# Performance work log

Hardware: AMD Instinct MI355X
Metric: run time of the kernel (lower is better)

## Reference

```python
import jax, jax.numpy as jnp
import numpy as np

GROUPS = 16
HEADS = 8
GN_EPS = 1e-5
L2_EPS = 1e-12


def setup_inputs() -> dict:
    key = jax.random.key(0)
    ks = jax.random.split(key, 8)
    B, C, H, W = 16, 256, 64, 64
    cg = C // GROUPS  # 16
    x = jax.random.normal(ks[0], (B, C, H, W), dtype=jnp.float32)
    # conv1x1 on grouped channels (has bias by default in nn.Conv2d)
    w_conv1x1 = jax.random.normal(ks[1], (cg, cg), dtype=jnp.float32) * 0.1
    b_conv1x1 = jax.random.normal(ks[2], (cg,), dtype=jnp.float32) * 0.01
    # GroupNorm(cg, cg) affine params
    gn_w = jnp.ones((cg,), dtype=jnp.float32)
    gn_b = jnp.zeros((cg,), dtype=jnp.float32)
    # qkv 1x1 conv (bias=False): [3C, C]
    w_qkv = jax.random.normal(ks[3], (3 * C, C), dtype=jnp.float32) * 0.05
    # project_out 1x1 conv (bias=False): [C, C]
    w_proj = jax.random.normal(ks[4], (C, C), dtype=jnp.float32) * 0.05
    temperature = jnp.ones((HEADS, 1, 1), dtype=jnp.float32)
    return {"x": x, "w_conv1x1": w_conv1x1, "b_conv1x1": b_conv1x1,
            "gn_w": gn_w, "gn_b": gn_b, "w_qkv": w_qkv, "w_proj": w_proj,
            "temperature": temperature}


def _forward(x, w_conv1x1, b_conv1x1, gn_w, gn_b, w_qkv, w_proj, temperature):
    b, c, h, w = x.shape
    g, cg = GROUPS, x.shape[1] // GROUPS
    gx = x.reshape(b * g, cg, h, w)

    # --- coordinate-attention gating branch ---
    x_h = gx.mean(axis=3)                      # [bg, cg, h]
    x_w = gx.mean(axis=2)                      # [bg, cg, w]
    cat = jnp.concatenate([x_h, x_w], axis=2)  # [bg, cg, h+w]
    hw_feat = jnp.einsum('oi,bil->bol', w_conv1x1, cat) + b_conv1x1[None, :, None]
    xh, xw = hw_feat[:, :, :h], hw_feat[:, :, h:]
    x1 = jax.nn.sigmoid(xh)[:, :, :, None] * jax.nn.sigmoid(xw)[:, :, None, :]  # [bg,cg,h,w]
    # GroupNorm(cg, cg) == per-channel normalization over (h, w)
    mu = x1.mean(axis=(2, 3), keepdims=True)
    var = x1.var(axis=(2, 3), keepdims=True)
    x1 = (x1 - mu) * jax.lax.rsqrt(var + GN_EPS)
    x1 = x1 * gn_w[None, :, None, None] + gn_b[None, :, None, None]
    # softmax over channels of global avg pool -> [bg, cg]
    x11 = jax.nn.softmax(x1.mean(axis=(2, 3)), axis=-1)

    # --- normalized channel (Restormer-style) attention ---
    n = h * w
    qkv = jnp.einsum('oi,bin->bon', w_qkv, x.reshape(b, c, n))  # [b, 3c, n]
    q, k, v = jnp.split(qkv, 3, axis=1)
    ch = c // HEADS
    q = q.reshape(b, HEADS, ch, n)
    k = k.reshape(b, HEADS, ch, n)
    v = v.reshape(b, HEADS, ch, n)
    q = q / jnp.maximum(jnp.linalg.norm(q, axis=-1, keepdims=True), L2_EPS)
    k = k / jnp.maximum(jnp.linalg.norm(k, axis=-1, keepdims=True), L2_EPS)
    attn = jnp.einsum('bhcn,bhdn->bhcd', q, k) * temperature[None]  # [b,H,ch,ch]
    attn = jax.nn.softmax(attn, axis=-1)
    out = jnp.einsum('bhcd,bhdn->bhcn', attn, v).reshape(b, c, n)
    out = jnp.einsum('oi,bin->bon', w_proj, out).reshape(b, c, h, w)

    # --- sigmoid-gated residual combine ---
    x12 = out.reshape(b * g, cg, n)
    weights = jnp.einsum('bc,bcn->bn', x11, x12).reshape(b * g, 1, h, w)
    return (gx * jax.nn.sigmoid(weights)).reshape(b, c, h, w) + out


def reference(x, w_conv1x1, b_conv1x1, gn_w, gn_b, w_qkv, w_proj, temperature):
    return _forward(x, w_conv1x1, b_conv1x1, gn_w, gn_b, w_qkv, w_proj, temperature)
```

## Files before the change

kernel.cpp:

```cpp
#include <hip/hip_runtime.h>
#include <math.h>


__device__ __forceinline__ float sigmoidf_(float v) { return 1.0f / (1.0f + __expf(-v)); }

typedef _Float16 half8 __attribute__((ext_vector_type(8)));
typedef _Float16 half4 __attribute__((ext_vector_type(4)));
typedef float f32x4 __attribute__((ext_vector_type(4)));

#define GLOAD_LDS16(gp, lp)                                                     \
    __builtin_amdgcn_global_load_lds(                                           \
        (const __attribute__((address_space(1))) void*)(gp),                    \
        (__attribute__((address_space(3))) void*)(lp), 16, 0, 0)

__global__ __launch_bounds__(256) void prep_fused(
    const float* __restrict__ X, _Float16* __restrict__ Xh, _Float16* __restrict__ Xt)
{
    __shared__ float tl[64][68];
    const int b = blockIdx.z, c0 = blockIdx.y * 64, n0 = blockIdx.x * 64;
    const int t = threadIdx.x;
    const int r0 = t >> 4;
    const int q = (t & 15) * 4;
    const float* Xb = X + ((long)b * 256 + c0) * 4096 + n0;
    _Float16* Xhb = Xh + ((long)b * 256 + c0) * 4096 + n0;
    #pragma unroll
    for (int i = 0; i < 4; ++i) {
        const int r = r0 + i * 16;
        const float4 v = *(const float4*)(Xb + (long)r * 4096 + q);
        tl[r][q + 0] = v.x; tl[r][q + 1] = v.y;
        tl[r][q + 2] = v.z; tl[r][q + 3] = v.w;
        half4 h = { (_Float16)v.x, (_Float16)v.y, (_Float16)v.z, (_Float16)v.w };
        *(half4*)(Xhb + (long)r * 4096 + q) = h;
    }
    __syncthreads();
    const int nn = t >> 2, cc = (t & 3) * 16;
    _Float16* Xtb = Xt + ((long)b * 4096 + n0 + nn) * 256 + c0 + cc;
    half8 o0, o1;
    #pragma unroll
    for (int k = 0; k < 8; ++k) o0[k] = (_Float16)tl[cc + k][nn];
    #pragma unroll
    for (int k = 0; k < 8; ++k) o1[k] = (_Float16)tl[cc + 8 + k][nn];
    *(half8*)(Xtb) = o0;
    *(half8*)(Xtb + 8) = o1;
}

__global__ __launch_bounds__(256) void cvt_half(const float* __restrict__ in,
                                                _Float16* __restrict__ o)
{
    const long i = ((long)blockIdx.x * 256 + threadIdx.x) * 4;
    const float4 v = *(const float4*)(in + i);
    half4 h = { (_Float16)v.x, (_Float16)v.y, (_Float16)v.z, (_Float16)v.w };
    *(half4*)(o + i) = h;
}

__global__ __launch_bounds__(256) void gram_split(const _Float16* __restrict__ Xh,
                                                  float* __restrict__ pG)
{
    __shared__ _Float16 Al[128 * 32];
    __shared__ _Float16 Bl[128 * 32];
    const int hw = blockIdx.x + 2 * blockIdx.y + 4 * blockIdx.z;
    const int f  = (hw & 7) * 64 + (hw >> 3);
    const int bx = f & 1, by = (f >> 1) & 1, bz = f >> 2;
    const int b = bz >> 3, s = bz & 7;
    const int m0 = by * 128, n0 = bx * 128;
    const _Float16* Xb = Xh + (long)b * 256 * 4096;
    const int t = threadIdx.x, lane = t & 63, wv = t >> 6;
    const int wm = (wv >> 1) * 64, wn = (wv & 1) * 64;
    f32x4 acc[4][4] = {};

    const int kbeg = s * 512, kend = kbeg + 512;
    for (int k0 = kbeg; k0 < kend; k0 += 32) {
        __syncthreads();
        #pragma unroll
        for (int r = 0; r < 2; ++r) {
            const int e = (r * 256 + t) * 8;
            const int row = e >> 5, col = e & 31;
            GLOAD_LDS16(Xb + (long)(m0 + row) * 4096 + k0 + col, &Al[e]);
            GLOAD_LDS16(Xb + (long)(n0 + row) * 4096 + k0 + col, &Bl[e]);
        }
        __syncthreads();
        half8 af[4], bf[4];
        #pragma unroll
        for (int ff = 0; ff < 4; ++ff) {
            af[ff] = *(const half8*)&Al[(wm + ff * 16 + (lane & 15)) * 32 + (lane >> 4) * 8];
            bf[ff] = *(const half8*)&Bl[(wn + ff * 16 + (lane & 15)) * 32 + (lane >> 4) * 8];
        }
        #pragma unroll
        for (int i = 0; i < 4; ++i)
            #pragma unroll
            for (int j = 0; j < 4; ++j)
                acc[i][j] = __builtin_amdgcn_mfma_f32_16x16x32_f16(af[i], bf[j], acc[i][j], 0, 0, 0);
    }
    float* pGb = pG + (long)s * 1048576 + (long)b * 65536;
    #pragma unroll
    for (int i = 0; i < 4; ++i)
        #pragma unroll
        for (int j = 0; j < 4; ++j) {
            const int row = m0 + wm + i * 16 + (lane >> 4) * 4;
            const int col = n0 + wn + j * 16 + (lane & 15);
            float* gp = pGb + (long)row * 256 + col;
            #pragma unroll
            for (int r = 0; r < 4; ++r) gp[(long)r * 256] = acc[i][j][r];
        }
}

__global__ __launch_bounds__(256) void reduce_g(const float* __restrict__ pG,
                                                _Float16* __restrict__ Gh)
{
    const long i = ((long)blockIdx.x * 256 + threadIdx.x) * 4;
    f32x4 s = {};
    #pragma unroll
    for (int k = 0; k < 8; ++k) {
        const float4 v = *(const float4*)(pG + (long)k * 1048576 + i);
        s[0] += v.x; s[1] += v.y; s[2] += v.z; s[3] += v.w;
    }
    half4 h = { (_Float16)s[0], (_Float16)s[1], (_Float16)s[2], (_Float16)s[3] };
    *(half4*)(Gh + i) = h;
}

template <bool DIAG, bool F16OUT>
__global__ __launch_bounds__(256) void mfma_bt(
    const _Float16* __restrict__ A, const _Float16* __restrict__ B,
    float* __restrict__ Cf, _Float16* __restrict__ Ch,
    long sA, long sB, long sC)
{
    __shared__ _Float16 Al[128 * 32];
    __shared__ _Float16 Bl[128 * 32];
    const int b = blockIdx.z;
    const int m0 = blockIdx.y * 128;
    const int n0 = DIAG ? m0 : blockIdx.x * 128;
    const _Float16* Ab = A + (long)b * sA;
    const _Float16* Bb = B + (long)b * sB;
    const int t = threadIdx.x, lane = t & 63, wv = t >> 6;
    const int wm = (wv >> 1) * 64, wn = (wv & 1) * 64;
    f32x4 acc[4][4] = {};

    for (int k0 = 0; k0 < 256; k0 += 32) {
        __syncthreads();
        #pragma unroll
        for (int r = 0; r < 2; ++r) {
            const int e = (r * 256 + t) * 8;
            const int row = e >> 5, col = e & 31;
            GLOAD_LDS16(Ab + (long)(m0 + row) * 256 + k0 + col, &Al[e]);
            GLOAD_LDS16(Bb + (long)(n0 + row) * 256 + k0 + col, &Bl[e]);
        }
        __syncthreads();
        half8 af[4], bf[4];
        #pragma unroll
        for (int ff = 0; ff < 4; ++ff) {
            af[ff] = *(const half8*)&Al[(wm + ff * 16 + (lane & 15)) * 32 + (lane >> 4) * 8];
            bf[ff] = *(const half8*)&Bl[(wn + ff * 16 + (lane & 15)) * 32 + (lane >> 4) * 8];
        }
        #pragma unroll
        for (int i = 0; i < 4; ++i)
            #pragma unroll
            for (int j = 0; j < 4; ++j)
                acc[i][j] = __builtin_amdgcn_mfma_f32_16x16x32_f16(af[i], bf[j], acc[i][j], 0, 0, 0);
    }
    #pragma unroll
    for (int i = 0; i < 4; ++i)
        #pragma unroll
        for (int j = 0; j < 4; ++j) {
            const int row = m0 + wm + i * 16 + (lane >> 4) * 4;
            const int col = n0 + wn + j * 16 + (lane & 15);
            #pragma unroll
            for (int r = 0; r < 4; ++r) {
                if (F16OUT)
                    Ch[(long)b * sC + (long)(row + r) * 256 + col] = (_Float16)acc[i][j][r];
                else
                    Cf[(long)b * sC + (long)(row + r) * 256 + col] = acc[i][j][r];
            }
        }
}

__global__ __launch_bounds__(256) void snorm_kernel(
    const _Float16* __restrict__ Th, const _Float16* __restrict__ wqkvh,
    float* __restrict__ Qn)
{
    const int gw = (int)((blockIdx.x * 256 + threadIdx.x) >> 6);
    const int lane = threadIdx.x & 63;
    const int b = gw >> 9, r = gw & 511;
    const half4 a = *(const half4*)(Th + (long)b * 131072 + (long)r * 256 + lane * 4);
    const half4 w = *(const half4*)(wqkvh + (long)r * 256 + lane * 4);
    float s = (float)a[0] * (float)w[0] + (float)a[1] * (float)w[1]
            + (float)a[2] * (float)w[2] + (float)a[3] * (float)w[3];
    #pragma unroll
    for (int off = 32; off; off >>= 1) s += __shfl_xor(s, off, 64);
    if (lane == 0) Qn[(long)b * 512 + r] = s;
}

__global__ __launch_bounds__(256) void attn2_kernel(
    const float* __restrict__ S1, const float* __restrict__ Qn,
    const float* __restrict__ wqkv, const float* __restrict__ temp,
    _Float16* __restrict__ MmT)
{
    const int bh = blockIdx.x;
    const int b = bh >> 3, h = bh & 7;
    const int t = threadIdx.x;
    __shared__ float pa[32][36];
    __shared__ float qn[32], kn[32];

    {
        const int r = t >> 3, c4 = (t & 7) * 4;
        const float4 v = *(const float4*)(
            S1 + (long)b * 65536 + (long)(h * 32 + r) * 256 + h * 32 + c4);
        pa[r][c4 + 0] = v.x; pa[r][c4 + 1] = v.y;
        pa[r][c4 + 2] = v.z; pa[r][c4 + 3] = v.w;
    }
    if (t < 32)
        qn[t] = fmaxf(sqrtf(Qn[(long)b * 512 + h * 32 + t]), 1e-12f);
    else if (t < 64)
        kn[t - 32] = fmaxf(sqrtf(Qn[(long)b * 512 + 256 + h * 32 + (t - 32)]), 1e-12f);
    __syncthreads();

    if (t < 32) {
        const float qin = temp[h] / qn[t];
        float lg[32];
        float mx = -1e30f;
        #pragma unroll
        for (int d = 0; d < 32; ++d) {
            const float l = pa[t][d] * qin / kn[d];
            lg[d] = l;
            mx = fmaxf(mx, l);
        }
        float s = 0.f;
        #pragma unroll
        for (int d = 0; d < 32; ++d) { lg[d] = __expf(lg[d] - mx); s += lg[d]; }
        const float inv = 1.0f / s;
        #pragma unroll
        for (int d = 0; d < 32; ++d) pa[t][d] = lg[d] * inv;
    }
    __syncthreads();

    float accm[32];
    #pragma unroll
    for (int c = 0; c < 32; ++c) accm[c] = 0.f;
    const float* wvp = wqkv + (long)(512 + h * 32) * 256 + t;
    #pragma unroll 4
    for (int d = 0; d < 32; ++d) {
        const float wvv = wvp[(long)d * 256];
        #pragma unroll
        for (int c = 0; c < 32; ++c) accm[c] += pa[c][d] * wvv;
    }
    _Float16* mo = MmT + (long)b * 65536 + (long)t * 256 + h * 32;
    #pragma unroll
    for (int c = 0; c < 32; ++c) mo[c] = (_Float16)accm[c];
}

__global__ __launch_bounds__(256) void w2h_kernel(
    const _Float16* __restrict__ Ph, const float* __restrict__ gnb,
    _Float16* __restrict__ W2)
{
    const int b = blockIdx.x, i = threadIdx.x;
    float e[16];
    float mx = -1e30f;
    #pragma unroll
    for (int c = 0; c < 16; ++c) mx = fmaxf(mx, gnb[c]);
    float s = 0.f;
    #pragma unroll
    for (int c = 0; c < 16; ++c) { e[c] = __expf(gnb[c] - mx); s += e[c]; }
    const float inv = 1.0f / s;
    const _Float16* Pb = Ph + (long)b * 65536 + i;
    #pragma unroll
    for (int g = 0; g < 16; ++g) {
        float acc = 0.f;
        #pragma unroll
        for (int c = 0; c < 16; ++c) acc += e[c] * (float)Pb[(long)(g * 16 + c) * 256];
        W2[((long)b * 16 + g) * 256 + i] = (_Float16)(acc * inv);
    }
}

__global__ __launch_bounds__(256) void out_fused(
    const _Float16* __restrict__ Ph, const _Float16* __restrict__ Xt,
    const _Float16* __restrict__ Xh, const _Float16* __restrict__ W2h,
    float* __restrict__ out)
{
    __shared__ __align__(16) char smem[40960];
    float (*cst)[128] = (float(*)[128])smem;
    float (*S2l)[128] = (float(*)[128])(smem + 32768);

    const int hw = blockIdx.x + 32 * blockIdx.y + 64 * blockIdx.z;
    const int f  = (hw & 7) * 128 + (hw >> 3);
    const int bx = f & 31, by = (f >> 5) & 1, bz = f >> 6;

    const int b = bz;
    const int m0 = by * 128, n0 = bx * 128;
    const _Float16* Ab = Ph + (long)b * 65536;
    const _Float16* Bb = Xt + (long)b * 1048576;
    const _Float16* W2b = W2h + (long)b * 4096;
    const int t = threadIdx.x, lane = t & 63, wv = t >> 6;
    const int wm = (wv >> 1) * 64, wn = (wv & 1) * 64;

    f32x4 acc[4][4] = {};
    f32x4 s2acc[4] = {};

#define OF_STAGE(P, K0) do {                                                     \
        _Float16* Al_ = (_Float16*)(smem + (P) * 16384);                         \
        _Float16* Bl_ = (_Float16*)(smem + (P) * 16384 + 8192);                  \
        _Pragma("unroll")                                                        \
        for (int r_ = 0; r_ < 2; ++r_) {                                         \
            const int e_ = (r_ * 256 + t) * 8;                                   \
            const int row_ = e_ >> 5, col_ = e_ & 31;                            \
            GLOAD_LDS16(Ab + (long)(m0 + row_) * 256 + (K0) + col_, &Al_[e_]);   \
            GLOAD_LDS16(Bb + (long)(n0 + row_) * 256 + (K0) + col_, &Bl_[e_]);   \
        } } while (0)

    OF_STAGE(0, 0);
    __syncthreads();
    int cur = 0;
    for (int ks = 0; ks < 8; ++ks) {
        if (ks < 7) OF_STAGE(cur ^ 1, (ks + 1) * 32);
        const int k0 = ks * 32;
        const half8 wf = *(const half8*)(W2b + (long)(lane & 15) * 256 + k0 + (lane >> 4) * 8);
        const _Float16* Al = (const _Float16*)(smem + cur * 16384);
        const _Float16* Bl = (const _Float16*)(smem + cur * 16384 + 8192);
        half8 af[4], bf[4];
        #pragma unroll
        for (int ff = 0; ff < 4; ++ff) {
            af[ff] = *(const half8*)&Al[(wm + ff * 16 + (lane & 15)) * 32 + (lane >> 4) * 8];
            bf[ff] = *(const half8*)&Bl[(wn + ff * 16 + (lane & 15)) * 32 + (lane >> 4) * 8];
        }
        #pragma unroll
        for (int i = 0; i < 4; ++i)
            #pragma unroll
            for (int j = 0; j < 4; ++j)
                acc[i][j] = __builtin_amdgcn_mfma_f32_16x16x32_f16(af[i], bf[j], acc[i][j], 0, 0, 0);
        #pragma unroll
        for (int j = 0; j < 4; ++j)
            s2acc[j] = __builtin_amdgcn_mfma_f32_16x16x32_f16(wf, bf[j], s2acc[j], 0, 0, 0);
        __syncthreads();
        cur ^= 1;
    }
#undef OF_STAGE

    if (wm == 0) {
        #pragma unroll
        for (int j = 0; j < 4; ++j)
            #pragma unroll
            for (int r = 0; r < 4; ++r)
                S2l[(lane >> 4) * 4 + r][wn + j * 16 + (lane & 15)] = s2acc[j][r];
    }

    const _Float16* Xhb = Xh + (long)b * 1048576;
    float* ob = out + (long)b * 1048576;

    #pragma unroll
    for (int hf = 0; hf < 2; ++hf) {
        if (wm == hf * 64) {
            #pragma unroll
            for (int i = 0; i < 4; ++i)
                #pragma unroll
                for (int j = 0; j < 4; ++j)
                    #pragma unroll
                    for (int r = 0; r < 4; ++r)
                        cst[i * 16 + (lane >> 4) * 4 + r][wn + j * 16 + (lane & 15)] = acc[i][j][r];
        }
        __syncthreads();
        #pragma unroll
        for (int it = 0; it < 8; ++it) {
            const int row = it * 8 + (t >> 5);
            const int col = (t & 31) * 4;
            const int c = m0 + hf * 64 + row;
            const float4 v = *(const float4*)&cst[row][col];
            const float4 s2 = *(const float4*)&S2l[c >> 4][col];
            const half4 xv = *(const half4*)(Xhb + (long)c * 4096 + n0 + col);
            float4 o;
            o.x = (float)xv[0] * sigmoidf_(s2.x) + v.x;
            o.y = (float)xv[1] * sigmoidf_(s2.y) + v.y;
            o.z = (float)xv[2] * sigmoidf_(s2.z) + v.z;
            o.w = (float)xv[3] * sigmoidf_(s2.w) + v.w;
            *(float4*)(ob + (long)c * 4096 + n0 + col) = o;
        }
        __syncthreads();
    }
}

template <bool BT, bool EPI>
__global__ __launch_bounds__(256) void gemm64(
    const float* __restrict__ A, const float* __restrict__ B, float* __restrict__ C,
    int M, int N, int K, long sA, long sB, long sC,
    const float* __restrict__ X, const float* __restrict__ WP)
{
    __shared__ float As[32][68];
    __shared__ float Bs[32][68];
    const int b = blockIdx.z;
    const float* Ab = A + (long)b * sA;
    const float* Bb = B + (long)b * sB;
    float* Cb = C + (long)b * sC;
    const int t = threadIdx.x;
    const int tx = t & 15, ty = t >> 4;
    const int m0 = blockIdx.y * 64, n0 = blockIdx.x * 64;

    float acc[4][4] = {};

    for (int k0 = 0; k0 < K; k0 += 32) {
        __syncthreads();
        #pragma unroll
        for (int f0 = 0; f0 < 512; f0 += 256) {
            const int f1 = f0 + t;
            const int row = f1 >> 3, c4 = f1 & 7;
            const float4 v = *(const float4*)(Ab + (long)(m0 + row) * K + k0 + c4 * 4);
            As[c4 * 4 + 0][row] = v.x;
            As[c4 * 4 + 1][row] = v.y;
            As[c4 * 4 + 2][row] = v.z;
            As[c4 * 4 + 3][row] = v.w;
        }
        if (BT) {
            #pragma unroll
            for (int f0 = 0; f0 < 512; f0 += 256) {
                const int f1 = f0 + t;
                const int row = f1 >> 3, c4 = f1 & 7;
                const float4 v = *(const float4*)(Bb + (long)(n0 + row) * K + k0 + c4 * 4);
                Bs[c4 * 4 + 0][row] = v.x;
                Bs[c4 * 4 + 1][row] = v.y;
                Bs[c4 * 4 + 2][row] = v.z;
                Bs[c4 * 4 + 3][row] = v.w;
            }
        } else {
            #pragma unroll
            for (int f0 = 0; f0 < 512; f0 += 256) {
                const int f1 = f0 + t;
                const int kk = f1 >> 4, c4 = f1 & 15;
                *(float4*)&Bs[kk][c4 * 4] =
                    *(const float4*)(Bb + (long)(k0 + kk) * N + n0 + c4 * 4);
            }
        }
        __syncthreads();
        #pragma unroll
        for (int kk = 0; kk < 32; ++kk) {
            const float4 av = *(const float4*)&As[kk][ty * 4];
            const float4 bv = *(const float4*)&Bs[kk][tx * 4];
            const float a0 = av.x, a1 = av.y, a2 = av.z, a3 = av.w;
            const float b0 = bv.x, b1 = bv.y, b2 = bv.z, b3 = bv.w;
            acc[0][0] += a0 * b0; acc[0][1] += a0 * b1; acc[0][2] += a0 * b2; acc[0][3] += a0 * b3;
            acc[1][0] += a1 * b0; acc[1][1] += a1 * b1; acc[1][2] += a1 * b2; acc[1][3] += a1 * b3;
            acc[2][0] += a2 * b0; acc[2][1] += a2 * b1; acc[2][2] += a2 * b2; acc[2][3] += a2 * b3;
            acc[3][0] += a3 * b0; acc[3][1] += a3 * b1; acc[3][2] += a3 * b2; acc[3][3] += a3 * b3;
        }
    }

    if (EPI) {
        #pragma unroll
        for (int i = 0; i < 4; ++i) {
            const int c = m0 + ty * 4 + i;
            const long nidx = n0 + tx * 4;
            const float4 xv = *(const float4*)(X + ((long)b * 256 + c) * 4096 + nidx);
            const float4 wv = *(const float4*)(WP + ((long)b * 16 + (c >> 4)) * 4096 + nidx);
            float4 o;
            o.x = xv.x * sigmoidf_(wv.x) + acc[i][0];
            o.y = xv.y * sigmoidf_(wv.y) + acc[i][1];
            o.z = xv.z * sigmoidf_(wv.z) + acc[i][2];
            o.w = xv.w * sigmoidf_(wv.w) + acc[i][3];
            *(float4*)(Cb + (long)c * N + nidx) = o;
        }
    } else {
        #pragma unroll
        for (int i = 0; i < 4; ++i) {
            const float4 o = make_float4(acc[i][0], acc[i][1], acc[i][2], acc[i][3]);
            *(float4*)(Cb + (long)(m0 + ty * 4 + i) * N + n0 + tx * 4) = o;
        }
    }
}

__global__ __launch_bounds__(256) void attn_kernel(
    const float* __restrict__ T, const float* __restrict__ wqkv,
    const float* __restrict__ temp, float* __restrict__ Mout, long tStride)
{
    const int bh = blockIdx.x;
    const int b = bh >> 3, h = bh & 7;
    const int t = threadIdx.x;
    __shared__ float Tq[32][260];
    __shared__ float qk[32][33];
    __shared__ float qn[32], kn[32];
    const float* Tb = T + (long)b * tStride;

    for (int f = t; f < 32 * 64; f += 256) {
        const int r = f >> 6, c4 = f & 63;
        *(float4*)&Tq[r][c4 * 4] = *(const float4*)(Tb + (long)(h * 32 + r) * 256 + c4 * 4);
    }
    __syncthreads();

    if (t < 32) {
        float s = 0.f;
        const float* wq = wqkv + (long)(h * 32 + t) * 256;
        #pragma unroll 4
        for (int k = 0; k < 256; k += 4) {
            const float4 a = *(const float4*)&Tq[t][k];
            const float4 w = *(const float4*)(wq + k);
            s += a.x * w.x + a.y * w.y + a.z * w.z + a.w * w.w;
        }
        qn[t] = fmaxf(sqrtf(s), 1e-12f);
    } else if (t < 64) {
        const int d = t - 32;
        float s = 0.f;
        const float* tk = Tb + (long)(256 + h * 32 + d) * 256;
        const float* wk = wqkv + (long)(256 + h * 32 + d) * 256;
        #pragma unroll 4
        for (int k = 0; k < 256; k += 4) {
            const float4 a = *(const float4*)(tk + k);
            const float4 w = *(const float4*)(wk + k);
            s += a.x * w.x + a.y * w.y + a.z * w.z + a.w * w.w;
        }
        kn[d] = fmaxf(sqrtf(s), 1e-12f);
    }

    {
        const int c = t >> 3, d0 = (t & 7) * 4;
        float s0 = 0, s1 = 0, s2 = 0, s3 = 0;
        const float* wk0 = wqkv + (long)(256 + h * 32 + d0) * 256;
        #pragma unroll 4
        for (int k = 0; k < 256; k += 4) {
            const float4 a = *(const float4*)&Tq[c][k];
            const float4 w0 = *(const float4*)(wk0 + k);
            const float4 w1 = *(const float4*)(wk0 + 256 + k);
            const float4 w2 = *(const float4*)(wk0 + 512 + k);
            const float4 w3 = *(const float4*)(wk0 + 768 + k);
            s0 += a.x * w0.x + a.y * w0.y + a.z * w0.z + a.w * w0.w;
            s1 += a.x * w1.x + a.y * w1.y + a.z * w1.z + a.w * w1.w;
            s2 += a.x * w2.x + a.y * w2.y + a.z * w2.z + a.w * w2.w;
            s3 += a.x * w3.x + a.y * w3.y + a.z * w3.z + a.w * w3.w;
        }
        qk[c][d0 + 0] = s0;
        qk[c][d0 + 1] = s1;
        qk[c][d0 + 2] = s2;
        qk[c][d0 + 3] = s3;
    }
    __syncthreads();

    if (t < 32) {
        const float tscale = temp[h];
        const float qin = tscale / qn[t];
        float lg[32];
        float mx = -1e30f;
        #pragma unroll
        for (int d = 0; d < 32; ++d) {
            const float l = qk[t][d] * qin / kn[d];
            lg[d] = l;
            mx = fmaxf(mx, l);
        }
        float s = 0.f;
        #pragma unroll
        for (int d = 0; d < 32; ++d) { lg[d] = __expf(lg[d] - mx); s += lg[d]; }
        const float inv = 1.0f / s;
        #pragma unroll
        for (int d = 0; d < 32; ++d) qk[t][d] = lg[d] * inv;
    }
    __syncthreads();

    float accm[32];
    #pragma unroll
    for (int c = 0; c < 32; ++c) accm[c] = 0.f;
    const float* wvp = wqkv + (long)(512 + h * 32) * 256 + t;
    #pragma unroll 4
    for (int d = 0; d < 32; ++d) {
        const float wvv = wvp[(long)d * 256];
        #pragma unroll
        for (int c = 0; c < 32; ++c) accm[c] += qk[c][d] * wvv;
    }
    float* mo = Mout + (long)b * 256 * 256 + (long)(h * 32) * 256 + t;
    #pragma unroll
    for (int c = 0; c < 32; ++c) mo[(long)c * 256] = accm[c];
}

__global__ __launch_bounds__(256) void w2_kernel(
    const float* __restrict__ P, const float* __restrict__ gnb, float* __restrict__ W2)
{
    const int b = blockIdx.x, i = threadIdx.x;
    float e[16];
    float mx = -1e30f;
    #pragma unroll
    for (int c = 0; c < 16; ++c) mx = fmaxf(mx, gnb[c]);
    float s = 0.f;
    #pragma unroll
    for (int c = 0; c < 16; ++c) { e[c] = __expf(gnb[c] - mx); s += e[c]; }
    const float inv = 1.0f / s;
    const float* Pb = P + (long)b * 256 * 256 + i;
    #pragma unroll
    for (int g = 0; g < 16; ++g) {
        float acc = 0.f;
        #pragma unroll
        for (int c = 0; c < 16; ++c) acc += e[c] * Pb[(long)(g * 16 + c) * 256];
        W2[((long)b * 16 + g) * 256 + i] = acc * inv;
    }
}

__global__ __launch_bounds__(256) void wpre_kernel(
    const float* __restrict__ W2, const float* __restrict__ X, float* __restrict__ WP)
{
    __shared__ float w2s[16][260];
    const int b = blockIdx.y;
    const int n = blockIdx.x * 256 + threadIdx.x;
    for (int f = threadIdx.x; f < 16 * 64; f += 256) {
        const int g = f >> 6, c4 = f & 63;
        *(float4*)&w2s[g][c4 * 4] = *(const float4*)(W2 + ((long)b * 16 + g) * 256 + c4 * 4);
    }
    __syncthreads();
    float acc[16] = {};
    const float* xb = X + (long)b * 256 * 4096 + n;
    for (int k = 0; k < 256; ++k) {
        const float xv = xb[(long)k * 4096];
        #pragma unroll
        for (int g = 0; g < 16; ++g) acc[g] += w2s[g][k] * xv;
    }
    #pragma unroll
    for (int g = 0; g < 16; ++g) WP[((long)b * 16 + g) * 4096 + n] = acc[g];
}

extern "C" void kernel_launch(void* const* d_in, const int* in_sizes, int n_in,
                              void* d_out, int out_size, void* d_ws, size_t ws_size,
                              hipStream_t stream)
{
    const float* x     = (const float*)d_in[0];
    const float* gnb   = (const float*)d_in[4];
    const float* wqkv  = (const float*)d_in[5];
    const float* wproj = (const float*)d_in[6];
    const float* temp  = (const float*)d_in[7];
    float* out = (float*)d_out;

    if (ws_size >= 82051072ULL) {
        char* w = (char*)d_ws;
        _Float16* Xh = (_Float16*)w;
        _Float16* Xt = (_Float16*)(w + 33554432);
        float*    S1 = (float*)(w + 67108864);
        char*     pool = w + 71303168;
        _Float16* wqkvh  = (_Float16*)pool;
        _Float16* wprojh = (_Float16*)(pool + 393216);
        _Float16* Gh     = (_Float16*)(pool + 524288);
        _Float16* MmT    = (_Float16*)(pool + 524288);
        _Float16* Th     = (_Float16*)(pool + 2621440);
        float*    Qn     = (float*)(pool + 6815744);
        _Float16* Ph     = (_Float16*)(pool + 6848512);
        _Float16* W2h    = (_Float16*)(pool + 8945664);
        float*    pG     = (float*)d_out;

        prep_fused<<<dim3(64, 4, 16), 256, 0, stream>>>(x, Xh, Xt);
        cvt_half<<<192, 256, 0, stream>>>(wqkv, wqkvh);
        cvt_half<<<64, 256, 0, stream>>>(wproj, wprojh);
        gram_split<<<dim3(2, 2, 128), 256, 0, stream>>>(Xh, pG);
        reduce_g<<<1024, 256, 0, stream>>>(pG, Gh);
        mfma_bt<false, true><<<dim3(2, 4, 16), 256, 0, stream>>>(
            wqkvh, Gh, nullptr, Th, 0L, 65536L, 131072L);
        snorm_kernel<<<2048, 256, 0, stream>>>(Th, wqkvh, Qn);
        mfma_bt<true, false><<<dim3(1, 2, 16), 256, 0, stream>>>(
            Th, wqkvh + 65536, S1, nullptr, 131072L, 0L, 65536L);
        attn2_kernel<<<128, 256, 0, stream>>>(S1, Qn, wqkv, temp, MmT);
        mfma_bt<false, true><<<dim3(2, 2, 16), 256, 0, stream>>>(
            wprojh, MmT, nullptr, Ph, 0L, 65536L, 65536L);
        w2h_kernel<<<16, 256, 0, stream>>>(Ph, gnb, W2h);
        out_fused<<<dim3(32, 2, 16), 256, 0, stream>>>(Ph, Xt, Xh, W2h, out);
    } else {
        float* ws = (float*)d_ws;
        float* G  = ws;
        float* T  = G  + 16L * 65536;
        float* Mm = T  + 16L * 196608;
        float* P  = Mm + 16L * 65536;
        float* W2 = P  + 16L * 65536;
        float* WP = W2 + 16L * 4096;

        gemm64<true, false><<<dim3(4, 4, 16), 256, 0, stream>>>(
            x, x, G, 256, 256, 4096, 1048576L, 1048576L, 65536L, nullptr, nullptr);
        gemm64<false, false><<<dim3(4, 12, 16), 256, 0, stream>>>(
            wqkv, G, T, 768, 256, 256, 0L, 65536L, 196608L, nullptr, nullptr);
        attn_kernel<<<128, 256, 0, stream>>>(T, wqkv, temp, Mm, 196608L);
        gemm64<false, false><<<dim3(4, 4, 16), 256, 0, stream>>>(
            wproj, Mm, P, 256, 256, 256, 0L, 65536L, 65536L, nullptr, nullptr);
        w2_kernel<<<16, 256, 0, stream>>>(P, gnb, W2);
        wpre_kernel<<<dim3(16, 16), 256, 0, stream>>>(W2, x, WP);
        gemm64<false, true><<<dim3(64, 4, 16), 256, 0, stream>>>(
            P, x, out, 256, 4096, 256, 65536L, 1048576L, 1048576L, x, WP);
    }
}
```

Before: 123.3 us.

## Exploit Gram symmetry, merge weight casts, fold norm calc into attention kernel

The Gram split kernel now computes only three of the four 128x128 tiles, since X·Xᵀ is symmetric, and a new mirror kernel fills the missing lower-left block by transposing the upper-right one. The two weight conversion launches are merged into one, and the separate q/k squared-norm kernel is removed; attn2 now computes those norms itself from Th and the half-precision weights. The final output uses nontemporal stores. Together these cut Gram MFMA work by a quarter and drop launches, at the cost of an extra small transpose launch and more work per attention block.

Measured after the change: 121.4 us. About the same (-1.5%).

```diff
diff --git a/kernel.cpp b/kernel.cpp
--- a/kernel.cpp
+++ b/kernel.cpp
@@ -44,13 +44,22 @@
     *(half8*)(Xtb + 8) = o1;
 }
 
-__global__ __launch_bounds__(256) void cvt_half(const float* __restrict__ in,
-                                                _Float16* __restrict__ o)
-{
-    const long i = ((long)blockIdx.x * 256 + threadIdx.x) * 4;
-    const float4 v = *(const float4*)(in + i);
-    half4 h = { (_Float16)v.x, (_Float16)v.y, (_Float16)v.z, (_Float16)v.w };
-    *(half4*)(o + i) = h;
+__global__ __launch_bounds__(256) void cvt_weights(
+    const float* __restrict__ wqkv, const float* __restrict__ wproj,
+    _Float16* __restrict__ wqkvh, _Float16* __restrict__ wprojh)
+{
+    const int blk = blockIdx.x;
+    if (blk < 192) {
+        const long i = ((long)blk * 256 + threadIdx.x) * 4;
+        const float4 v = *(const float4*)(wqkv + i);
+        half4 h = { (_Float16)v.x, (_Float16)v.y, (_Float16)v.z, (_Float16)v.w };
+        *(half4*)(wqkvh + i) = h;
+    } else {
+        const long i = ((long)(blk - 192) * 256 + threadIdx.x) * 4;
+        const float4 v = *(const float4*)(wproj + i);
+        half4 h = { (_Float16)v.x, (_Float16)v.y, (_Float16)v.z, (_Float16)v.w };
+        *(half4*)(wprojh + i) = h;
+    }
 }
 
 __global__ __launch_bounds__(256) void gram_split(const _Float16* __restrict__ Xh,
@@ -58,11 +67,13 @@
 {
     __shared__ _Float16 Al[128 * 32];
     __shared__ _Float16 Bl[128 * 32];
-    const int hw = blockIdx.x + 2 * blockIdx.y + 4 * blockIdx.z;
-    const int f  = (hw & 7) * 64 + (hw >> 3);
-    const int bx = f & 1, by = (f >> 1) & 1, bz = f >> 2;
+    const int hw = blockIdx.x + 3 * blockIdx.y;
+    const int f  = (hw & 7) * 48 + (hw >> 3);
+    const int tile = f % 3;
+    const int bz = f / 3;
     const int b = bz >> 3, s = bz & 7;
-    const int m0 = by * 128, n0 = bx * 128;
+    const int m0 = (tile == 1) ? 128 : 0;
+    const int n0 = (tile == 0) ? 0 : 128;
     const _Float16* Xb = Xh + (long)b * 256 * 4096;
     const int t = threadIdx.x, lane = t & 63, wv = t >> 6;
     const int wm = (wv >> 1) * 64, wn = (wv & 1) * 64;
@@ -116,6 +127,25 @@
     }
     half4 h = { (_Float16)s[0], (_Float16)s[1], (_Float16)s[2], (_Float16)s[3] };
     *(half4*)(Gh + i) = h;
+}
+
+__global__ __launch_bounds__(256) void mirror_g(_Float16* __restrict__ Gh)
+{
+    __shared__ _Float16 tl[64][72];
+    const int b = blockIdx.z, r0 = 128 + blockIdx.y * 64, c0 = blockIdx.x * 64;
+    const int t = threadIdx.x;
+    const int ii = t >> 2, jj = (t & 3) * 16;
+    _Float16* Gb = Gh + (long)b * 65536;
+    *(half8*)&tl[ii][jj]     = *(const half8*)(Gb + (long)(c0 + ii) * 256 + r0 + jj);
+    *(half8*)&tl[ii][jj + 8] = *(const half8*)(Gb + (long)(c0 + ii) * 256 + r0 + jj + 8);
+    __syncthreads();
+    half8 o0, o1;
+    #pragma unroll
+    for (int k = 0; k < 8; ++k) o0[k] = tl[jj + k][ii];
+    #pragma unroll
+    for (int k = 0; k < 8; ++k) o1[k] = tl[jj + 8 + k][ii];
+    *(half8*)(Gb + (long)(r0 + ii) * 256 + c0 + jj) = o0;
+    *(half8*)(Gb + (long)(r0 + ii) * 256 + c0 + jj + 8) = o1;
 }
 
 template <bool DIAG, bool F16OUT>
@@ -173,26 +203,10 @@
         }
 }
 
-__global__ __launch_bounds__(256) void snorm_kernel(
-    const _Float16* __restrict__ Th, const _Float16* __restrict__ wqkvh,
-    float* __restrict__ Qn)
-{
-    const int gw = (int)((blockIdx.x * 256 + threadIdx.x) >> 6);
-    const int lane = threadIdx.x & 63;
-    const int b = gw >> 9, r = gw & 511;
-    const half4 a = *(const half4*)(Th + (long)b * 131072 + (long)r * 256 + lane * 4);
-    const half4 w = *(const half4*)(wqkvh + (long)r * 256 + lane * 4);
-    float s = (float)a[0] * (float)w[0] + (float)a[1] * (float)w[1]
-            + (float)a[2] * (float)w[2] + (float)a[3] * (float)w[3];
-    #pragma unroll
-    for (int off = 32; off; off >>= 1) s += __shfl_xor(s, off, 64);
-    if (lane == 0) Qn[(long)b * 512 + r] = s;
-}
-
 __global__ __launch_bounds__(256) void attn2_kernel(
-    const float* __restrict__ S1, const float* __restrict__ Qn,
-    const float* __restrict__ wqkv, const float* __restrict__ temp,
-    _Float16* __restrict__ MmT)
+    const float* __restrict__ S1, const _Float16* __restrict__ Th,
+    const _Float16* __restrict__ wqkvh, const float* __restrict__ wqkv,
+    const float* __restrict__ temp, _Float16* __restrict__ MmT)
 {
     const int bh = blockIdx.x;
     const int b = bh >> 3, h = bh & 7;
@@ -207,10 +221,26 @@
         pa[r][c4 + 0] = v.x; pa[r][c4 + 1] = v.y;
         pa[r][c4 + 2] = v.z; pa[r][c4 + 3] = v.w;
     }
-    if (t < 32)
-        qn[t] = fmaxf(sqrtf(Qn[(long)b * 512 + h * 32 + t]), 1e-12f);
-    else if (t < 64)
-        kn[t - 32] = fmaxf(sqrtf(Qn[(long)b * 512 + 256 + h * 32 + (t - 32)]), 1e-12f);
+    {
+        const int r = t >> 2, q = t & 3;
+        const long rrow = (r < 32) ? (long)(h * 32 + r) : (long)(256 + h * 32 + (r - 32));
+        const _Float16* ta = Th + (long)b * 131072 + rrow * 256 + q * 64;
+        const _Float16* wa = wqkvh + rrow * 256 + q * 64;
+        float s = 0.f;
+        #pragma unroll
+        for (int k = 0; k < 64; k += 4) {
+            const half4 a = *(const half4*)(ta + k);
+            const half4 w = *(const half4*)(wa + k);
+            s += (float)a[0] * (float)w[0] + (float)a[1] * (float)w[1]
+               + (float)a[2] * (float)w[2] + (float)a[3] * (float)w[3];
+        }
+        s += __shfl_xor(s, 1, 64);
+        s += __shfl_xor(s, 2, 64);
+        if (q == 0) {
+            const float v = fmaxf(sqrtf(s), 1e-12f);
+            if (r < 32) qn[r] = v; else kn[r - 32] = v;
+        }
+    }
     __syncthreads();
 
     if (t < 32) {
@@ -364,12 +394,12 @@
             const float4 v = *(const float4*)&cst[row][col];
             const float4 s2 = *(const float4*)&S2l[c >> 4][col];
             const half4 xv = *(const half4*)(Xhb + (long)c * 4096 + n0 + col);
-            float4 o;
-            o.x = (float)xv[0] * sigmoidf_(s2.x) + v.x;
-            o.y = (float)xv[1] * sigmoidf_(s2.y) + v.y;
-            o.z = (float)xv[2] * sigmoidf_(s2.z) + v.z;
-            o.w = (float)xv[3] * sigmoidf_(s2.w) + v.w;
-            *(float4*)(ob + (long)c * 4096 + n0 + col) = o;
+            f32x4 o;
+            o[0] = (float)xv[0] * sigmoidf_(s2.x) + v.x;
+            o[1] = (float)xv[1] * sigmoidf_(s2.y) + v.y;
+            o[2] = (float)xv[2] * sigmoidf_(s2.z) + v.z;
+            o[3] = (float)xv[3] * sigmoidf_(s2.w) + v.w;
+            __builtin_nontemporal_store(o, (f32x4*)(ob + (long)c * 4096 + n0 + col));
         }
         __syncthreads();
     }
@@ -628,22 +658,20 @@
         _Float16* Gh     = (_Float16*)(pool + 524288);
         _Float16* MmT    = (_Float16*)(pool + 524288);
         _Float16* Th     = (_Float16*)(pool + 2621440);
-        float*    Qn     = (float*)(pool + 6815744);
         _Float16* Ph     = (_Float16*)(pool + 6848512);
         _Float16* W2h    = (_Float16*)(pool + 8945664);
         float*    pG     = (float*)d_out;
 
         prep_fused<<<dim3(64, 4, 16), 256, 0, stream>>>(x, Xh, Xt);
-        cvt_half<<<192, 256, 0, stream>>>(wqkv, wqkvh);
-        cvt_half<<<64, 256, 0, stream>>>(wproj, wprojh);
-        gram_split<<<dim3(2, 2, 128), 256, 0, stream>>>(Xh, pG);
+        cvt_weights<<<256, 256, 0, stream>>>(wqkv, wproj, wqkvh, wprojh);
+        gram_split<<<dim3(3, 128), 256, 0, stream>>>(Xh, pG);
         reduce_g<<<1024, 256, 0, stream>>>(pG, Gh);
+        mirror_g<<<dim3(2, 2, 16), 256, 0, stream>>>(Gh);
         mfma_bt<false, true><<<dim3(2, 4, 16), 256, 0, stream>>>(
             wqkvh, Gh, nullptr, Th, 0L, 65536L, 131072L);
-        snorm_kernel<<<2048, 256, 0, stream>>>(Th, wqkvh, Qn);
         mfma_bt<true, false><<<dim3(1, 2, 16), 256, 0, stream>>>(
             Th, wqkvh + 65536, S1, nullptr, 131072L, 0L, 65536L);
-        attn2_kernel<<<128, 256, 0, stream>>>(S1, Qn, wqkv, temp, MmT);
+        attn2_kernel<<<128, 256, 0, stream>>>(S1, Th, wqkvh, wqkv, temp, MmT);
         mfma_bt<false, true><<<dim3(2, 2, 16), 256, 0, stream>>>(
             wprojh, MmT, nullptr, Ph, 0L, 65536L, 65536L);
         w2h_kernel<<<16, 256, 0, stream>>>(Ph, gnb, W2h);
```
